# Optimization experiments

Hardware: AMD Instinct MI355X
Metric: run time of the kernel (lower is better)

## Reference

```python
import jax, jax.numpy as jnp
import numpy as np

# dims
N, E, B, T = 1024, 8192, 4, 8          # nodes, edges, batch, time steps
IN, HID, H, NCLASS = 64, 64, 4, 7      # in_dim, nhidden, heads, nclass
K = N - NCLASS + 1                     # output-head conv width
NEG, EPS = 0.2, 1e-5


def setup_inputs() -> dict:
    key = jax.random.key(0)
    ks = jax.random.split(key, 24)
    p = lambda i, shape: jax.random.normal(ks[i], shape, jnp.float32) * 0.05
    inputs = jax.random.normal(ks[0], (B, IN, T, N), jnp.float32)
    src = jax.random.randint(ks[1], (E,), 0, N, jnp.int32)
    dst = jnp.repeat(jnp.arange(N, dtype=jnp.int32), E // N)  # every node has in-degree 8
    return {
        "inputs": inputs, "src": src, "dst": dst,
        "W0": p(2, (H * HID, IN)), "al0": p(3, (H, HID)), "ar0": p(4, (H, HID)),
        "W1": p(5, (H * HID, H * HID)), "al1": p(6, (H, HID)), "ar1": p(7, (H, HID)),
        "W2": p(8, (H * 1, H * HID)), "al2": p(9, (H, 1)), "ar2": p(10, (H, 1)),
        "Wres2": p(11, (H * 1, H * HID)),
        # Outputlayer
        "tc1_w": p(12, (H, H, T)), "tc1_b": p(13, (H,)),
        "ln1_g": jnp.ones((N, H), jnp.float32), "ln1_b": jnp.zeros((N, H), jnp.float32),
        "tc2_w": p(14, (1, H)), "tc2_b": p(15, (1,)),
        "ln2_g": jnp.ones((N, 1), jnp.float32), "ln2_b": jnp.zeros((N, 1), jnp.float32),
        "fc_w": p(16, (K,)), "fc_b": p(17, (1,)),
    }


def _gat_conv(h, src, dst, W, al, ar, res=None, act=None):
    # h: (N,B,T,F) -> feat: (N,B,T,H,D)
    heads, d = al.shape
    feat = (h @ W.T).reshape(N, B, T, heads, d)
    el = jnp.einsum('nbthd,hd->nbth', feat, al)
    er = jnp.einsum('nbthd,hd->nbth', feat, ar)
    e = jax.nn.leaky_relu(el[src] + er[dst], NEG)           # (E,B,T,H)
    emax = jax.ops.segment_max(e, dst, num_segments=N)
    ex = jnp.exp(e - emax[dst])
    den = jax.ops.segment_sum(ex, dst, num_segments=N)
    a = ex / den[dst]                                        # edge softmax over incoming edges
    out = jax.ops.segment_sum(feat[src] * a[..., None], dst, num_segments=N)  # (N,B,T,H,D)
    if res is not None:
        out = out + res
    if act is not None:
        out = act(out)
    return out


def reference(inputs, src, dst,
              W0, al0, ar0, W1, al1, ar1, W2, al2, ar2, Wres2,
              tc1_w, tc1_b, ln1_g, ln1_b, tc2_w, tc2_b, ln2_g, ln2_b, fc_w, fc_b):
    # (B,IN,T,N) -> (N,B,T,IN) : transpose(0,3).transpose(1,3)
    h = jnp.transpose(inputs.astype(jnp.float32), (3, 0, 2, 1))
    h1 = _gat_conv(h, src, dst, W0, al0, ar0, act=jax.nn.elu).reshape(N, B, T, H * HID)
    h2 = _gat_conv(h1, src, dst, W1, al1, ar1,
                   res=h1.reshape(N, B, T, H, HID), act=jax.nn.elu).reshape(N, B, T, H * HID)
    res2 = (h2 @ Wres2.T).reshape(N, B, T, H, 1)
    o = _gat_conv(h2, src, dst, W2, al2, ar2, res=res2)      # (N,B,T,H,1)
    # transpose(1,3).transpose(0,3).squeeze(-1) -> (B,H,T,N)
    x = jnp.transpose(o[..., 0], (1, 3, 2, 0))

    # Outputlayer
    # tconv1: Conv2d(H->H, kernel (T,1)) collapses time -> (B,H,N)
    x1 = jnp.einsum('oht,bhtn->bon', tc1_w, x) + tc1_b[None, :, None]
    # ln1: LayerNorm over (N,H) of (B,1,N,H)
    z = jnp.transpose(x1, (0, 2, 1))                          # (B,N,H)
    mu = z.mean(axis=(1, 2), keepdims=True)
    var = z.var(axis=(1, 2), keepdims=True)
    z = (z - mu) / jnp.sqrt(var + EPS) * ln1_g + ln1_b
    x1 = jnp.transpose(z, (0, 2, 1))                          # (B,H,N)
    # tconv2: 1x1 conv H->1 -> (B,1,N)
    x2 = jnp.einsum('oh,bhn->bon', tc2_w, x1) + tc2_b[None, :, None]
    # ln2: LayerNorm over (N,1)
    mu = x2.mean(axis=2, keepdims=True)
    var = x2.var(axis=2, keepdims=True)
    x2 = (x2 - mu) / jnp.sqrt(var + EPS) * ln2_g[:, 0] + ln2_b[:, 0]
    # fc: Conv2d(1->1, kernel (1,K)) sliding over nodes -> (B,NCLASS)
    xc = x2[:, :, None, :]                                    # (B,1,1,N) NCHW
    w = fc_w[None, None, None, :]                             # (1,1,1,K) OIHW
    out = jax.lax.conv_general_dilated(xc, w, (1, 1), 'VALID') + fc_b[None, :, None, None]
    return out[:, 0, 0, :]                                    # (B, NCLASS)
```

## Files before the change

### kernel.cpp

```cpp
#include <hip/hip_runtime.h>
#include <math.h>

#define NEGS 0.2f
#define EPSF 1e-5f

typedef short s16x8 __attribute__((ext_vector_type(8)));
typedef float f32x4 __attribute__((ext_vector_type(4)));

__device__ __forceinline__ float b2f(unsigned short u) {
  union { unsigned int i; float f; } v; v.i = ((unsigned int)u) << 16; return v.f;
}
__device__ __forceinline__ unsigned short f2b(float f) {
  union { float f; unsigned int i; } v; v.f = f;
  unsigned int x = v.i;
  return (unsigned short)((x + 0x7fffu + ((x >> 16) & 1u)) >> 16);
}

__device__ __forceinline__ float block_reduce1024(float v, float* red) {
  #pragma unroll
  for (int o = 32; o > 0; o >>= 1) v += __shfl_down(v, o);
  __syncthreads();
  if ((threadIdx.x & 63) == 0) red[threadIdx.x >> 6] = v;
  __syncthreads();
  float s = 0.f;
  #pragma unroll
  for (int i = 0; i < 16; ++i) s += red[i];
  return s;
}

__global__ __launch_bounds__(256) void k_feat0(
    const float* __restrict__ inp, const float* __restrict__ W0,
    const float* __restrict__ W1, const float* __restrict__ al,
    const float* __restrict__ ar, unsigned short* __restrict__ feat,
    float* __restrict__ el, float* __restrict__ er,
    unsigned short* __restrict__ W1b)
{
  const int tid = threadIdx.x;
  if (blockIdx.x >= 512) {
    const int j = (blockIdx.x - 512) * 256 + tid;
    float4 w4 = *(const float4*)&W1[j*4];
    ushort4 o4; o4.x=f2b(w4.x); o4.y=f2b(w4.y); o4.z=f2b(w4.z); o4.w=f2b(w4.w);
    *(ushort4*)&W1b[j*4] = o4;
    return;
  }
  __shared__ __align__(16) unsigned short At[64][72];
  __shared__ __align__(16) unsigned short Lb[64*256];
  const int g  = blockIdx.x & 7;
  const int bt = g*4 + ((blockIdx.x >> 3) & 3);
  const int n0 = (blockIdx.x >> 5) * 64;
  const int b  = bt >> 3, t = bt & 7;
  const int w    = tid >> 6;
  const int lane = tid & 63;
  const int n16  = lane & 15;
  const int q    = lane >> 4;
  s16x8 bf[2][4];
  #pragma unroll
  for (int kc = 0; kc < 2; ++kc)
    #pragma unroll
    for (int ct = 0; ct < 4; ++ct) {
      const float* p = &W0[(size_t)((w*4 + ct)*16 + n16)*64 + kc*32 + q*8];
      float4 wa = *(const float4*)p;
      float4 wb = *(const float4*)(p + 4);
      s16x8 o;
      o[0]=(short)f2b(wa.x); o[1]=(short)f2b(wa.y); o[2]=(short)f2b(wa.z); o[3]=(short)f2b(wa.w);
      o[4]=(short)f2b(wb.x); o[5]=(short)f2b(wb.y); o[6]=(short)f2b(wb.z); o[7]=(short)f2b(wb.w);
      bf[kc][ct] = o;
    }
  {
    const int nn = tid & 63, cg = tid >> 6;
    #pragma unroll
    for (int c2 = 0; c2 < 8; ++c2) {
      int ch = (cg*8 + c2) * 2;
      float vx = inp[((size_t)(b*64 + ch  )*8 + t)*1024 + n0 + nn];
      float vy = inp[((size_t)(b*64 + ch+1)*8 + t)*1024 + n0 + nn];
      unsigned int pk = ((unsigned int)f2b(vy) << 16) | (unsigned int)f2b(vx);
      *(unsigned int*)&At[nn][ch] = pk;
    }
  }
  __syncthreads();
  f32x4 acc[4][4];
  #pragma unroll
  for (int rt = 0; rt < 4; ++rt)
    #pragma unroll
    for (int ct = 0; ct < 4; ++ct) acc[rt][ct] = (f32x4){0.f,0.f,0.f,0.f};
  #pragma unroll
  for (int kc = 0; kc < 2; ++kc) {
    s16x8 af[4];
    #pragma unroll
    for (int rt = 0; rt < 4; ++rt)
      af[rt] = *(const s16x8*)&At[rt*16 + n16][kc*32 + q*8];
    #pragma unroll
    for (int rt = 0; rt < 4; ++rt)
      #pragma unroll
      for (int ct = 0; ct < 4; ++ct)
        acc[rt][ct] = __builtin_amdgcn_mfma_f32_16x16x32_bf16(af[rt], bf[kc][ct], acc[rt][ct], 0, 0, 0);
  }
  float alv[4], arv[4];
  #pragma unroll
  for (int ct = 0; ct < 4; ++ct) {
    alv[ct] = al[w*64 + ct*16 + n16];
    arv[ct] = ar[w*64 + ct*16 + n16];
  }
  #pragma unroll
  for (int rt = 0; rt < 4; ++rt) {
    #pragma unroll
    for (int reg = 0; reg < 4; ++reg) {
      float pl = acc[rt][0][reg]*alv[0] + acc[rt][1][reg]*alv[1]
               + acc[rt][2][reg]*alv[2] + acc[rt][3][reg]*alv[3];
      float pr = acc[rt][0][reg]*arv[0] + acc[rt][1][reg]*arv[1]
               + acc[rt][2][reg]*arv[2] + acc[rt][3][reg]*arv[3];
      #pragma unroll
      for (int o = 1; o < 16; o <<= 1) { pl += __shfl_xor(pl, o); pr += __shfl_xor(pr, o); }
      if (n16 == 0) {
        int r = (n0 + rt*16 + q*4 + reg)*32 + bt;
        el[r*4 + w] = pl;
        er[r*4 + w] = pr;
      }
    }
  }
  #pragma unroll
  for (int rt = 0; rt < 4; ++rt)
    #pragma unroll
    for (int ct = 0; ct < 4; ++ct)
      #pragma unroll
      for (int reg = 0; reg < 4; ++reg)
        Lb[(rt*16 + q*4 + reg)*256 + w*64 + ct*16 + n16] = f2b(acc[rt][ct][reg]);
  __syncthreads();
  #pragma unroll
  for (int i = 0; i < 8; ++i) {
    int u = tid + i*256;
    int m = u >> 5, off = (u & 31) * 8;
    *(s16x8*)&feat[(size_t)((n0 + m)*32 + bt)*256 + off] = *(const s16x8*)&Lb[m*256 + off];
  }
}

__global__ __launch_bounds__(256, 4) void k_agg0_feat1(
    const unsigned short* __restrict__ feat0, const float* __restrict__ el0,
    const float* __restrict__ er0, const int* __restrict__ src,
    const unsigned short* __restrict__ W1b, const float* __restrict__ al,
    const float* __restrict__ ar, unsigned short* __restrict__ h1b,
    unsigned short* __restrict__ feat1, float* __restrict__ el1, float* __restrict__ er1)
{
  __shared__ float wsm[32][8][4];
  __shared__ int   ssm[32][8];
  __shared__ __align__(16) unsigned short smbuf[32*264];
  unsigned short (*At)[264] = (unsigned short(*)[264])smbuf;
  unsigned short *Lb = smbuf;
  const int tid = threadIdx.x;
  const int g     = blockIdx.x & 7;
  const int bt    = g*4 + ((blockIdx.x >> 3) & 3);
  const int nBase = (blockIdx.x >> 5) * 32;
  ((int*)ssm)[tid] = src[nBase*8 + tid];
  __syncthreads();
  if (tid < 128) {
    const int nl = tid >> 2, h = tid & 3;
    const int rn = (nBase + nl)*32 + bt;
    const float erv = er0[rn*4 + h];
    float e[8]; float mx = -1e30f;
    #pragma unroll
    for (int j = 0; j < 8; ++j) {
      float v = el0[(ssm[nl][j]*32 + bt)*4 + h] + erv;
      v = v >= 0.f ? v : NEGS * v;
      e[j] = v; mx = fmaxf(mx, v);
    }
    float den = 0.f;
    #pragma unroll
    for (int j = 0; j < 8; ++j) { e[j] = __expf(e[j] - mx); den += e[j]; }
    const float inv = 1.f / den;
    #pragma unroll
    for (int j = 0; j < 8; ++j) wsm[nl][j][h] = e[j] * inv;
  }
  __syncthreads();
  {
    const int hw2 = tid >> 5, l5 = tid & 31;
    const int c0 = l5 * 8, hh = l5 >> 3;
    #pragma unroll
    for (int p2 = 0; p2 < 2; ++p2) {
      const int nlA = p2*16 + hw2, nlB = nlA + 8;
      s16x8 vA[8], vB[8];
      #pragma unroll
      for (int j = 0; j < 8; ++j) {
        vA[j] = *(const s16x8*)&feat0[(size_t)(ssm[nlA][j]*32 + bt)*256 + c0];
        vB[j] = *(const s16x8*)&feat0[(size_t)(ssm[nlB][j]*32 + bt)*256 + c0];
      }
      asm volatile("" ::: "memory");
      float aA[8] = {0,0,0,0,0,0,0,0}, aB[8] = {0,0,0,0,0,0,0,0};
      #pragma unroll
      for (int j = 0; j < 8; ++j) {
        const float wA = wsm[nlA][j][hh], wB = wsm[nlB][j][hh];
        #pragma unroll
        for (int i = 0; i < 8; ++i) {
          aA[i] = fmaf(wA, b2f((unsigned short)vA[j][i]), aA[i]);
          aB[i] = fmaf(wB, b2f((unsigned short)vB[j][i]), aB[i]);
        }
      }
      s16x8 oA, oB;
      #pragma unroll
      for (int i = 0; i < 8; ++i) {
        float xA = aA[i] > 0.f ? aA[i] : expm1f(aA[i]);
        float xB = aB[i] > 0.f ? aB[i] : expm1f(aB[i]);
        oA[i] = (short)f2b(xA); oB[i] = (short)f2b(xB);
      }
      *(s16x8*)&At[nlA][c0] = oA;
      *(s16x8*)&At[nlB][c0] = oB;
      *(s16x8*)&h1b[(size_t)((nBase + nlA)*32 + bt)*256 + c0] = oA;
      *(s16x8*)&h1b[(size_t)((nBase + nlB)*32 + bt)*256 + c0] = oB;
    }
  }
  __syncthreads();
  const int w    = tid >> 6;
  const int lane = tid & 63;
  const int n16  = lane & 15;
  const int q    = lane >> 4;
  f32x4 acc[2][4];
  #pragma unroll
  for (int rt = 0; rt < 2; ++rt)
    #pragma unroll
    for (int ct = 0; ct < 4; ++ct) acc[rt][ct] = (f32x4){0.f,0.f,0.f,0.f};
  #pragma unroll
  for (int kc = 0; kc < 8; ++kc) {
    s16x8 af[2], bfr[4];
    #pragma unroll
    for (int rt = 0; rt < 2; ++rt)
      af[rt] = *(const s16x8*)&At[rt*16 + n16][kc*32 + q*8];
    #pragma unroll
    for (int ct = 0; ct < 4; ++ct)
      bfr[ct] = *(const s16x8*)&W1b[(size_t)((w*4 + ct)*16 + n16)*256 + kc*32 + q*8];
    #pragma unroll
    for (int rt = 0; rt < 2; ++rt)
      #pragma unroll
      for (int ct = 0; ct < 4; ++ct)
        acc[rt][ct] = __builtin_amdgcn_mfma_f32_16x16x32_bf16(af[rt], bfr[ct], acc[rt][ct], 0, 0, 0);
  }
  float alv[4], arv[4];
  #pragma unroll
  for (int ct = 0; ct < 4; ++ct) {
    alv[ct] = al[w*64 + ct*16 + n16];
    arv[ct] = ar[w*64 + ct*16 + n16];
  }
  #pragma unroll
  for (int rt = 0; rt < 2; ++rt) {
    #pragma unroll
    for (int reg = 0; reg < 4; ++reg) {
      float pl = acc[rt][0][reg]*alv[0] + acc[rt][1][reg]*alv[1]
               + acc[rt][2][reg]*alv[2] + acc[rt][3][reg]*alv[3];
      float pr = acc[rt][0][reg]*arv[0] + acc[rt][1][reg]*arv[1]
               + acc[rt][2][reg]*arv[2] + acc[rt][3][reg]*arv[3];
      #pragma unroll
      for (int o = 1; o < 16; o <<= 1) { pl += __shfl_xor(pl, o); pr += __shfl_xor(pr, o); }
      if (n16 == 0) {
        int r = (nBase + rt*16 + q*4 + reg)*32 + bt;
        el1[r*4 + w] = pl;
        er1[r*4 + w] = pr;
      }
    }
  }
  __syncthreads();
  #pragma unroll
  for (int rt = 0; rt < 2; ++rt)
    #pragma unroll
    for (int ct = 0; ct < 4; ++ct)
      #pragma unroll
      for (int reg = 0; reg < 4; ++reg)
        Lb[(rt*16 + q*4 + reg)*256 + w*64 + ct*16 + n16] = f2b(acc[rt][ct][reg]);
  __syncthreads();
  #pragma unroll
  for (int i = 0; i < 4; ++i) {
    int u = tid + i*256;
    int row = u >> 5, off = (u & 31) * 8;
    *(s16x8*)&feat1[(size_t)((nBase + row)*32 + bt)*256 + off] = *(const s16x8*)&Lb[row*256 + off];
  }
}

__global__ __launch_bounds__(256, 4) void k_agg1_proj(
    const unsigned short* __restrict__ feat1, const float* __restrict__ el,
    const float* __restrict__ er, const int* __restrict__ src,
    const unsigned short* __restrict__ h1b, const float* __restrict__ W2,
    const float* __restrict__ Wres2, float* __restrict__ feat2, float* __restrict__ res2)
{
  __shared__ float wsm[32][8][4];
  __shared__ int   ssm[32][8];
  __shared__ __align__(16) float Wp[8][256];
  const int tid = threadIdx.x;
  const int g     = blockIdx.x & 7;
  const int bt    = g*4 + ((blockIdx.x >> 3) & 3);
  const int nBase = (blockIdx.x >> 5) * 32;
  ((int*)ssm)[tid] = src[nBase*8 + tid];
  for (int j2 = tid; j2 < 2048; j2 += 256) {
    int o = j2 >> 8, k = j2 & 255;
    Wp[o][k] = (o < 4) ? W2[o*256 + k] : Wres2[(o-4)*256 + k];
  }
  __syncthreads();
  if (tid < 128) {
    const int nl = tid >> 2, h = tid & 3;
    const int rn = (nBase + nl)*32 + bt;
    const float erv = er[rn*4 + h];
    float e[8]; float mx = -1e30f;
    #pragma unroll
    for (int j = 0; j < 8; ++j) {
      float v = el[(ssm[nl][j]*32 + bt)*4 + h] + erv;
      v = v >= 0.f ? v : NEGS * v;
      e[j] = v; mx = fmaxf(mx, v);
    }
    float den = 0.f;
    #pragma unroll
    for (int j = 0; j < 8; ++j) { e[j] = __expf(e[j] - mx); den += e[j]; }
    const float inv = 1.f / den;
    #pragma unroll
    for (int j = 0; j < 8; ++j) wsm[nl][j][h] = e[j] * inv;
  }
  __syncthreads();
  const int hw2 = tid >> 5, l5 = tid & 31;
  const int c0 = l5 * 8, hh = l5 >> 3;
  #pragma unroll
  for (int p2 = 0; p2 < 2; ++p2) {
    const int nlA = p2*16 + hw2, nlB = nlA + 8;
    const int rnA = (nBase + nlA)*32 + bt, rnB = (nBase + nlB)*32 + bt;
    s16x8 vA[8], vB[8], rrA, rrB;
    rrA = *(const s16x8*)&h1b[(size_t)rnA*256 + c0];
    rrB = *(const s16x8*)&h1b[(size_t)rnB*256 + c0];
    #pragma unroll
    for (int j = 0; j < 8; ++j) {
      vA[j] = *(const s16x8*)&feat1[(size_t)(ssm[nlA][j]*32 + bt)*256 + c0];
      vB[j] = *(const s16x8*)&feat1[(size_t)(ssm[nlB][j]*32 + bt)*256 + c0];
    }
    asm volatile("" ::: "memory");
    float aA[8] = {0,0,0,0,0,0,0,0}, aB[8] = {0,0,0,0,0,0,0,0};
    #pragma unroll
    for (int j = 0; j < 8; ++j) {
      const float wA = wsm[nlA][j][hh], wB = wsm[nlB][j][hh];
      #pragma unroll
      for (int i = 0; i < 8; ++i) {
        aA[i] = fmaf(wA, b2f((unsigned short)vA[j][i]), aA[i]);
        aB[i] = fmaf(wB, b2f((unsigned short)vB[j][i]), aB[i]);
      }
    }
    #pragma unroll
    for (int i = 0; i < 8; ++i) {
      float xA = aA[i] + b2f((unsigned short)rrA[i]);
      float xB = aB[i] + b2f((unsigned short)rrB[i]);
      aA[i] = xA > 0.f ? xA : expm1f(xA);
      aB[i] = xB > 0.f ? xB : expm1f(xB);
    }
    #pragma unroll
    for (int o = 0; o < 8; ++o) {
      float4 wa = *(const float4*)&Wp[o][c0];
      float4 wb = *(const float4*)&Wp[o][c0 + 4];
      float pA = aA[0]*wa.x + aA[1]*wa.y + aA[2]*wa.z + aA[3]*wa.w
               + aA[4]*wb.x + aA[5]*wb.y + aA[6]*wb.z + aA[7]*wb.w;
      float pB = aB[0]*wa.x + aB[1]*wa.y + aB[2]*wa.z + aB[3]*wa.w
               + aB[4]*wb.x + aB[5]*wb.y + aB[6]*wb.z + aB[7]*wb.w;
      #pragma unroll
      for (int off = 1; off < 32; off <<= 1) {
        pA += __shfl_xor(pA, off);
        pB += __shfl_xor(pB, off);
      }
      if (l5 == 0) {
        if (o < 4) { feat2[rnA*4 + o] = pA; feat2[rnB*4 + o] = pB; }
        else       { res2[rnA*4 + (o-4)] = pA; res2[rnB*4 + (o-4)] = pB; }
      }
    }
  }
}

__global__ __launch_bounds__(128) void k_agg2(
    const float* __restrict__ feat2, const float* __restrict__ res2,
    const int* __restrict__ src, const float* __restrict__ al2,
    const float* __restrict__ ar2, const float* __restrict__ tc1w,
    const float* __restrict__ tc1b, float* __restrict__ x1)
{
  __shared__ float os[4][8][4];
  const int n = blockIdx.x;
  const int tid = threadIdx.x;
  const int b = tid >> 5, t = (tid >> 2) & 7, h = tid & 3;
  const int rn = n*32 + b*8 + t;
  const float av = al2[h], rv = ar2[h];
  const float erv = feat2[rn*4 + h] * rv;
  float f[8], e[8]; float m = -1e30f;
  #pragma unroll
  for (int j = 0; j < 8; ++j) {
    int s_ = src[n*8 + j];
    f[j] = feat2[(s_*32 + b*8 + t)*4 + h];
    float v = f[j]*av + erv;
    v = v >= 0.f ? v : NEGS * v;
    e[j] = v; m = fmaxf(m, v);
  }
  float den = 0.f, num = 0.f;
  #pragma unroll
  for (int j = 0; j < 8; ++j) { float ex = __expf(e[j]-m); den += ex; num = fmaf(ex, f[j], num); }
  os[b][t][h] = num/den + res2[rn*4 + h];
  __syncthreads();
  if (tid < 16) {
    int b2 = tid >> 2, o2 = tid & 3;
    float acc = tc1b[o2];
    #pragma unroll
    for (int hh = 0; hh < 4; ++hh)
      #pragma unroll
      for (int tt = 0; tt < 8; ++tt)
        acc = fmaf(tc1w[(o2*4 + hh)*8 + tt], os[b2][tt][hh], acc);
    x1[(b2*4 + o2)*1024 + n] = acc;
  }
}

__global__ __launch_bounds__(1024) void k_final(
    const float* __restrict__ x1, const float* __restrict__ ln1g,
    const float* __restrict__ ln1b, const float* __restrict__ tc2w,
    const float* __restrict__ tc2b, const float* __restrict__ ln2g,
    const float* __restrict__ ln2b, const float* __restrict__ fcw,
    const float* __restrict__ fcb, float* __restrict__ out)
{
  __shared__ float red[16];
  __shared__ float x2s[1024];
  const int b = blockIdx.x;
  const int tid = threadIdx.x;
  float s = 0.f, q = 0.f;
  for (int j = tid; j < 4096; j += 1024) {
    float v = x1[b*4096 + j];
    s += v; q += v*v;
  }
  float S = block_reduce1024(s, red);
  float Q = block_reduce1024(q, red);
  float mu  = S * (1.f/4096.f);
  float var = Q * (1.f/4096.f) - mu*mu;
  float inv = rsqrtf(var + EPSF);
  float tb = tc2b[0];
  const int nn = tid;
  float acc = tb;
  #pragma unroll
  for (int h = 0; h < 4; ++h) {
    float z = (x1[b*4096 + h*1024 + nn] - mu) * inv * ln1g[nn*4 + h] + ln1b[nn*4 + h];
    acc = fmaf(tc2w[h], z, acc);
  }
  float S2 = block_reduce1024(acc, red);
  float Q2 = block_reduce1024(acc*acc, red);
  float mu2  = S2 * (1.f/1024.f);
  float inv2 = rsqrtf(Q2 * (1.f/1024.f) - mu2*mu2 + EPSF);
  x2s[nn] = (acc - mu2) * inv2 * ln2g[nn] + ln2b[nn];
  __syncthreads();
  for (int c = 0; c < 7; ++c) {
    float p = (tid < 1018) ? x2s[c + tid] * fcw[tid] : 0.f;
    float P = block_reduce1024(p, red);
    if (tid == 0) out[b*7 + c] = P + fcb[0];
  }
}

extern "C" void kernel_launch(void* const* d_in, const int* in_sizes, int n_in,
                              void* d_out, int out_size, void* d_ws, size_t ws_size,
                              hipStream_t stream)
{
  const float* inp  = (const float*)d_in[0];
  const int*   src  = (const int*)  d_in[1];
  const float* W0   = (const float*)d_in[3];
  const float* al0  = (const float*)d_in[4];
  const float* ar0  = (const float*)d_in[5];
  const float* W1   = (const float*)d_in[6];
  const float* al1  = (const float*)d_in[7];
  const float* ar1  = (const float*)d_in[8];
  const float* W2   = (const float*)d_in[9];
  const float* al2  = (const float*)d_in[10];
  const float* ar2  = (const float*)d_in[11];
  const float* Wr2  = (const float*)d_in[12];
  const float* tc1w = (const float*)d_in[13];
  const float* tc1b = (const float*)d_in[14];
  const float* ln1g = (const float*)d_in[15];
  const float* ln1b = (const float*)d_in[16];
  const float* tc2w = (const float*)d_in[17];
  const float* tc2b = (const float*)d_in[18];
  const float* ln2g = (const float*)d_in[19];
  const float* ln2b = (const float*)d_in[20];
  const float* fcw  = (const float*)d_in[21];
  const float* fcb  = (const float*)d_in[22];
  float* out = (float*)d_out;

  unsigned short* W1b    = (unsigned short*)d_ws;
  unsigned short* featb0 = W1b    + 65536;
  unsigned short* featb1 = featb0 + 8388608;
  unsigned short* h1b    = featb1 + 8388608;
  float* el0   = (float*)(h1b + 8388608);
  float* er0   = el0   + 131072;
  float* el1   = er0   + 131072;
  float* er1   = el1   + 131072;
  float* feat2 = er1   + 131072;
  float* res2  = feat2 + 131072;
  float* x1    = res2  + 131072;

  k_feat0<<<dim3(576), dim3(256), 0, stream>>>(inp, W0, W1, al0, ar0,
                                               featb0, el0, er0, W1b);
  k_agg0_feat1<<<dim3(1024), dim3(256), 0, stream>>>(featb0, el0, er0, src, W1b, al1, ar1,
                                                     h1b, featb1, el1, er1);
  k_agg1_proj<<<dim3(1024), dim3(256), 0, stream>>>(featb1, el1, er1, src, h1b, W2, Wr2,
                                                    feat2, res2);
  k_agg2<<<dim3(1024), dim3(128), 0, stream>>>(feat2, res2, src, al2, ar2, tc1w, tc1b, x1);
  k_final<<<dim3(4), dim3(1024), 0, stream>>>(x1, ln1g, ln1b, tc2w, tc2b, ln2g, ln2b, fcw, fcb, out);
}
```

Measured before the change: 170.7 us.

## Aggregate before projecting in GAT layers and fold attention vectors into weights

```diff
diff --git a/kernel.cpp b/kernel.cpp
--- a/kernel.cpp
+++ b/kernel.cpp
@@ -15,6 +15,7 @@
   unsigned int x = v.i;
   return (unsigned short)((x + 0x7fffu + ((x >> 16) & 1u)) >> 16);
 }
+__device__ __forceinline__ float eluf(float x) { return x > 0.f ? x : expm1f(x); }
 
 __device__ __forceinline__ float block_reduce1024(float v, float* red) {
   #pragma unroll
@@ -28,138 +29,154 @@
   return s;
 }
 
-__global__ __launch_bounds__(256) void k_feat0(
+__global__ __launch_bounds__(256) void k_pre(
     const float* __restrict__ inp, const float* __restrict__ W0,
-    const float* __restrict__ W1, const float* __restrict__ al,
-    const float* __restrict__ ar, unsigned short* __restrict__ feat,
-    float* __restrict__ el, float* __restrict__ er,
-    unsigned short* __restrict__ W1b)
+    const float* __restrict__ W1, const float* __restrict__ al0,
+    const float* __restrict__ ar0, const float* __restrict__ al1,
+    const float* __restrict__ ar1, unsigned short* __restrict__ Xb,
+    unsigned short* __restrict__ W0b, unsigned short* __restrict__ W1b,
+    float* __restrict__ vl0g, float* __restrict__ vr0g,
+    float* __restrict__ vl1g, float* __restrict__ vr1g)
 {
   const int tid = threadIdx.x;
+  if (blockIdx.x == 576) {
+    float accl1[4] = {0,0,0,0}, accr1[4] = {0,0,0,0};
+    #pragma unroll
+    for (int h = 0; h < 4; ++h)
+      for (int d = 0; d < 64; ++d) {
+        float w = W1[(size_t)(h*64 + d)*256 + tid];
+        accl1[h] = fmaf(w, al1[h*64 + d], accl1[h]);
+        accr1[h] = fmaf(w, ar1[h*64 + d], accr1[h]);
+      }
+    #pragma unroll
+    for (int h = 0; h < 4; ++h) { vl1g[h*256 + tid] = accl1[h]; vr1g[h*256 + tid] = accr1[h]; }
+    if (tid < 64) {
+      float accl0[4] = {0,0,0,0}, accr0[4] = {0,0,0,0};
+      for (int h = 0; h < 4; ++h)
+        for (int d = 0; d < 64; ++d) {
+          float w = W0[(h*64 + d)*64 + tid];
+          accl0[h] = fmaf(w, al0[h*64 + d], accl0[h]);
+          accr0[h] = fmaf(w, ar0[h*64 + d], accr0[h]);
+        }
+      for (int h = 0; h < 4; ++h) { vl0g[h*64 + tid] = accl0[h]; vr0g[h*64 + tid] = accr0[h]; }
+    }
+    return;
+  }
   if (blockIdx.x >= 512) {
     const int j = (blockIdx.x - 512) * 256 + tid;
+    W0b[j] = f2b(W0[j]);
     float4 w4 = *(const float4*)&W1[j*4];
     ushort4 o4; o4.x=f2b(w4.x); o4.y=f2b(w4.y); o4.z=f2b(w4.z); o4.w=f2b(w4.w);
     *(ushort4*)&W1b[j*4] = o4;
     return;
   }
-  __shared__ __align__(16) unsigned short At[64][72];
-  __shared__ __align__(16) unsigned short Lb[64*256];
-  const int g  = blockIdx.x & 7;
-  const int bt = g*4 + ((blockIdx.x >> 3) & 3);
-  const int n0 = (blockIdx.x >> 5) * 64;
-  const int b  = bt >> 3, t = bt & 7;
-  const int w    = tid >> 6;
-  const int lane = tid & 63;
-  const int n16  = lane & 15;
-  const int q    = lane >> 4;
-  s16x8 bf[2][4];
-  #pragma unroll
-  for (int kc = 0; kc < 2; ++kc)
-    #pragma unroll
-    for (int ct = 0; ct < 4; ++ct) {
-      const float* p = &W0[(size_t)((w*4 + ct)*16 + n16)*64 + kc*32 + q*8];
-      float4 wa = *(const float4*)p;
-      float4 wb = *(const float4*)(p + 4);
-      s16x8 o;
-      o[0]=(short)f2b(wa.x); o[1]=(short)f2b(wa.y); o[2]=(short)f2b(wa.z); o[3]=(short)f2b(wa.w);
-      o[4]=(short)f2b(wb.x); o[5]=(short)f2b(wb.y); o[6]=(short)f2b(wb.z); o[7]=(short)f2b(wb.w);
-      bf[kc][ct] = o;
-    }
-  {
-    const int nn = tid & 63, cg = tid >> 6;
-    #pragma unroll
-    for (int c2 = 0; c2 < 8; ++c2) {
-      int ch = (cg*8 + c2) * 2;
-      float vx = inp[((size_t)(b*64 + ch  )*8 + t)*1024 + n0 + nn];
-      float vy = inp[((size_t)(b*64 + ch+1)*8 + t)*1024 + n0 + nn];
-      unsigned int pk = ((unsigned int)f2b(vy) << 16) | (unsigned int)f2b(vx);
-      *(unsigned int*)&At[nn][ch] = pk;
-    }
-  }
-  __syncthreads();
-  f32x4 acc[4][4];
-  #pragma unroll
-  for (int rt = 0; rt < 4; ++rt)
-    #pragma unroll
-    for (int ct = 0; ct < 4; ++ct) acc[rt][ct] = (f32x4){0.f,0.f,0.f,0.f};
-  #pragma unroll
-  for (int kc = 0; kc < 2; ++kc) {
-    s16x8 af[4];
-    #pragma unroll
-    for (int rt = 0; rt < 4; ++rt)
-      af[rt] = *(const s16x8*)&At[rt*16 + n16][kc*32 + q*8];
-    #pragma unroll
-    for (int rt = 0; rt < 4; ++rt)
-      #pragma unroll
-      for (int ct = 0; ct < 4; ++ct)
-        acc[rt][ct] = __builtin_amdgcn_mfma_f32_16x16x32_bf16(af[rt], bf[kc][ct], acc[rt][ct], 0, 0, 0);
-  }
-  float alv[4], arv[4];
-  #pragma unroll
-  for (int ct = 0; ct < 4; ++ct) {
-    alv[ct] = al[w*64 + ct*16 + n16];
-    arv[ct] = ar[w*64 + ct*16 + n16];
-  }
-  #pragma unroll
-  for (int rt = 0; rt < 4; ++rt) {
-    #pragma unroll
-    for (int reg = 0; reg < 4; ++reg) {
-      float pl = acc[rt][0][reg]*alv[0] + acc[rt][1][reg]*alv[1]
-               + acc[rt][2][reg]*alv[2] + acc[rt][3][reg]*alv[3];
-      float pr = acc[rt][0][reg]*arv[0] + acc[rt][1][reg]*arv[1]
-               + acc[rt][2][reg]*arv[2] + acc[rt][3][reg]*arv[3];
-      #pragma unroll
-      for (int o = 1; o < 16; o <<= 1) { pl += __shfl_xor(pl, o); pr += __shfl_xor(pr, o); }
-      if (n16 == 0) {
-        int r = (n0 + rt*16 + q*4 + reg)*32 + bt;
-        el[r*4 + w] = pl;
-        er[r*4 + w] = pr;
-      }
-    }
-  }
-  #pragma unroll
-  for (int rt = 0; rt < 4; ++rt)
-    #pragma unroll
-    for (int ct = 0; ct < 4; ++ct)
-      #pragma unroll
-      for (int reg = 0; reg < 4; ++reg)
-        Lb[(rt*16 + q*4 + reg)*256 + w*64 + ct*16 + n16] = f2b(acc[rt][ct][reg]);
-  __syncthreads();
-  #pragma unroll
-  for (int i = 0; i < 8; ++i) {
-    int u = tid + i*256;
-    int m = u >> 5, off = (u & 31) * 8;
-    *(s16x8*)&feat[(size_t)((n0 + m)*32 + bt)*256 + off] = *(const s16x8*)&Lb[m*256 + off];
-  }
-}
-
-__global__ __launch_bounds__(256, 4) void k_agg0_feat1(
-    const unsigned short* __restrict__ feat0, const float* __restrict__ el0,
-    const float* __restrict__ er0, const int* __restrict__ src,
-    const unsigned short* __restrict__ W1b, const float* __restrict__ al,
-    const float* __restrict__ ar, unsigned short* __restrict__ h1b,
-    unsigned short* __restrict__ feat1, float* __restrict__ el1, float* __restrict__ er1)
+  __shared__ float L[64][65];
+  const int blk = blockIdx.x;
+  const int n0 = (blk & 15) * 64;
+  const int t  = (blk >> 4) & 7;
+  const int b  = blk >> 7;
+  const int nn = tid & 63, ch0 = tid >> 6;
+  #pragma unroll
+  for (int ch = ch0; ch < 64; ch += 4)
+    L[ch][nn] = inp[((size_t)(b*64 + ch)*8 + t)*1024 + n0 + nn];
+  __syncthreads();
+  const int r = tid >> 2, ck = tid & 3;
+  s16x8 o0, o1;
+  #pragma unroll
+  for (int i = 0; i < 8; ++i) o0[i] = (short)f2b(L[ck*16 + i][r]);
+  #pragma unroll
+  for (int i = 0; i < 8; ++i) o1[i] = (short)f2b(L[ck*16 + 8 + i][r]);
+  const int row = (n0 + r)*32 + b*8 + t;
+  *(s16x8*)&Xb[(size_t)row*64 + ck*16]     = o0;
+  *(s16x8*)&Xb[(size_t)row*64 + ck*16 + 8] = o1;
+}
+
+__global__ __launch_bounds__(256) void k_l0(
+    const unsigned short* __restrict__ Xb, const int* __restrict__ src,
+    const unsigned short* __restrict__ W0b, const float* __restrict__ vl0g,
+    const float* __restrict__ vr0g, const float* __restrict__ vl1g,
+    const float* __restrict__ vr1g, unsigned short* __restrict__ h1b,
+    float* __restrict__ el1, float* __restrict__ er1)
 {
-  __shared__ float wsm[32][8][4];
   __shared__ int   ssm[32][8];
-  __shared__ __align__(16) unsigned short smbuf[32*264];
-  unsigned short (*At)[264] = (unsigned short(*)[264])smbuf;
-  unsigned short *Lb = smbuf;
+  __shared__ __align__(16) float vl0s[4][64], vr0s[4][64];
+  __shared__ __align__(16) float vl1s[4][256], vr1s[4][256];
+  __shared__ float er0s[32][4];
+  __shared__ float el0s[32][8][4];
+  __shared__ float a_lds[32][33];
+  __shared__ __align__(16) unsigned short x_lds[32][8][72];
+  __shared__ __align__(16) unsigned short At[4][32][72];
+  __shared__ float elpart[4][32][4], erpart[4][32][4];
   const int tid = threadIdx.x;
   const int g     = blockIdx.x & 7;
   const int bt    = g*4 + ((blockIdx.x >> 3) & 3);
   const int nBase = (blockIdx.x >> 5) * 32;
+
   ((int*)ssm)[tid] = src[nBase*8 + tid];
-  __syncthreads();
+  ((float4*)vl1s)[tid] = ((const float4*)vl1g)[tid];
+  ((float4*)vr1s)[tid] = ((const float4*)vr1g)[tid];
+  if (tid < 64) {
+    ((float4*)vl0s)[tid] = ((const float4*)vl0g)[tid];
+    ((float4*)vr0s)[tid] = ((const float4*)vr0g)[tid];
+  }
+  __syncthreads();
+
+  {
+    const int nl = tid >> 3, j = tid & 7;
+    const unsigned short* xp = Xb + (size_t)(ssm[nl][j]*32 + bt)*64;
+    s16x8 xr[8];
+    #pragma unroll
+    for (int i = 0; i < 8; ++i) xr[i] = *(const s16x8*)&xp[i*8];
+    s16x8 xo = *(const s16x8*)&Xb[(size_t)((nBase + nl)*32 + bt)*64 + j*8];
+    asm volatile("" ::: "memory");
+    #pragma unroll
+    for (int h = 0; h < 4; ++h) {
+      float s = 0.f;
+      #pragma unroll
+      for (int i = 0; i < 8; ++i) {
+        f32x4 va = *(const f32x4*)&vl0s[h][i*8];
+        f32x4 vb = *(const f32x4*)&vl0s[h][i*8 + 4];
+        s = fmaf(b2f((unsigned short)xr[i][0]), va[0], s);
+        s = fmaf(b2f((unsigned short)xr[i][1]), va[1], s);
+        s = fmaf(b2f((unsigned short)xr[i][2]), va[2], s);
+        s = fmaf(b2f((unsigned short)xr[i][3]), va[3], s);
+        s = fmaf(b2f((unsigned short)xr[i][4]), vb[0], s);
+        s = fmaf(b2f((unsigned short)xr[i][5]), vb[1], s);
+        s = fmaf(b2f((unsigned short)xr[i][6]), vb[2], s);
+        s = fmaf(b2f((unsigned short)xr[i][7]), vb[3], s);
+      }
+      el0s[nl][j][h] = s;
+    }
+    float erp[4];
+    #pragma unroll
+    for (int h = 0; h < 4; ++h) {
+      f32x4 va = *(const f32x4*)&vr0s[h][j*8];
+      f32x4 vb = *(const f32x4*)&vr0s[h][j*8 + 4];
+      float s = b2f((unsigned short)xo[0])*va[0] + b2f((unsigned short)xo[1])*va[1]
+              + b2f((unsigned short)xo[2])*va[2] + b2f((unsigned short)xo[3])*va[3]
+              + b2f((unsigned short)xo[4])*vb[0] + b2f((unsigned short)xo[5])*vb[1]
+              + b2f((unsigned short)xo[6])*vb[2] + b2f((unsigned short)xo[7])*vb[3];
+      erp[h] = s;
+    }
+    #pragma unroll
+    for (int o = 1; o < 8; o <<= 1)
+      #pragma unroll
+      for (int h = 0; h < 4; ++h) erp[h] += __shfl_xor(erp[h], o);
+    if (j == 0)
+      #pragma unroll
+      for (int h = 0; h < 4; ++h) er0s[nl][h] = erp[h];
+    #pragma unroll
+    for (int i = 0; i < 8; ++i) *(s16x8*)&x_lds[nl][j][i*8] = xr[i];
+  }
+  __syncthreads();
+
   if (tid < 128) {
     const int nl = tid >> 2, h = tid & 3;
-    const int rn = (nBase + nl)*32 + bt;
-    const float erv = er0[rn*4 + h];
+    const float erv = er0s[nl][h];
     float e[8]; float mx = -1e30f;
     #pragma unroll
     for (int j = 0; j < 8; ++j) {
-      float v = el0[(ssm[nl][j]*32 + bt)*4 + h] + erv;
+      float v = el0s[nl][j][h] + erv;
       v = v >= 0.f ? v : NEGS * v;
       e[j] = v; mx = fmaxf(mx, v);
     }
@@ -168,46 +185,33 @@
     for (int j = 0; j < 8; ++j) { e[j] = __expf(e[j] - mx); den += e[j]; }
     const float inv = 1.f / den;
     #pragma unroll
-    for (int j = 0; j < 8; ++j) wsm[nl][j][h] = e[j] * inv;
-  }
-  __syncthreads();
-  {
-    const int hw2 = tid >> 5, l5 = tid & 31;
-    const int c0 = l5 * 8, hh = l5 >> 3;
-    #pragma unroll
-    for (int p2 = 0; p2 < 2; ++p2) {
-      const int nlA = p2*16 + hw2, nlB = nlA + 8;
-      s16x8 vA[8], vB[8];
+    for (int j = 0; j < 8; ++j) a_lds[nl][j*4 + h] = e[j] * inv;
+  }
+  __syncthreads();
+
+  {
+    const int nl = tid >> 3, ci = tid & 7;
+    s16x8 xv[8];
+    #pragma unroll
+    for (int j = 0; j < 8; ++j) xv[j] = *(const s16x8*)&x_lds[nl][j][ci*8];
+    #pragma unroll
+    for (int h = 0; h < 4; ++h) {
+      float acc8[8] = {0,0,0,0,0,0,0,0};
       #pragma unroll
       for (int j = 0; j < 8; ++j) {
-        vA[j] = *(const s16x8*)&feat0[(size_t)(ssm[nlA][j]*32 + bt)*256 + c0];
-        vB[j] = *(const s16x8*)&feat0[(size_t)(ssm[nlB][j]*32 + bt)*256 + c0];
-      }
-      asm volatile("" ::: "memory");
-      float aA[8] = {0,0,0,0,0,0,0,0}, aB[8] = {0,0,0,0,0,0,0,0};
-      #pragma unroll
-      for (int j = 0; j < 8; ++j) {
-        const float wA = wsm[nlA][j][hh], wB = wsm[nlB][j][hh];
-        #pragma unroll
-        for (int i = 0; i < 8; ++i) {
-          aA[i] = fmaf(wA, b2f((unsigned short)vA[j][i]), aA[i]);
-          aB[i] = fmaf(wB, b2f((unsigned short)vB[j][i]), aB[i]);
-        }
-      }
-      s16x8 oA, oB;
-      #pragma unroll
-      for (int i = 0; i < 8; ++i) {
-        float xA = aA[i] > 0.f ? aA[i] : expm1f(aA[i]);
-        float xB = aB[i] > 0.f ? aB[i] : expm1f(aB[i]);
-        oA[i] = (short)f2b(xA); oB[i] = (short)f2b(xB);
-      }
-      *(s16x8*)&At[nlA][c0] = oA;
-      *(s16x8*)&At[nlB][c0] = oB;
-      *(s16x8*)&h1b[(size_t)((nBase + nlA)*32 + bt)*256 + c0] = oA;
-      *(s16x8*)&h1b[(size_t)((nBase + nlB)*32 + bt)*256 + c0] = oB;
-    }
-  }
-  __syncthreads();
+        const float wa = a_lds[nl][j*4 + h];
+        #pragma unroll
+        for (int e = 0; e < 8; ++e)
+          acc8[e] = fmaf(wa, b2f((unsigned short)xv[j][e]), acc8[e]);
+      }
+      s16x8 o;
+      #pragma unroll
+      for (int e = 0; e < 8; ++e) o[e] = (short)f2b(acc8[e]);
+      *(s16x8*)&At[h][nl][ci*8] = o;
+    }
+  }
+  __syncthreads();
+
   const int w    = tid >> 6;
   const int lane = tid & 63;
   const int n16  = lane & 15;
@@ -218,69 +222,92 @@
     #pragma unroll
     for (int ct = 0; ct < 4; ++ct) acc[rt][ct] = (f32x4){0.f,0.f,0.f,0.f};
   #pragma unroll
-  for (int kc = 0; kc < 8; ++kc) {
+  for (int kc = 0; kc < 2; ++kc) {
     s16x8 af[2], bfr[4];
     #pragma unroll
     for (int rt = 0; rt < 2; ++rt)
-      af[rt] = *(const s16x8*)&At[rt*16 + n16][kc*32 + q*8];
+      af[rt] = *(const s16x8*)&At[w][rt*16 + n16][kc*32 + q*8];
     #pragma unroll
     for (int ct = 0; ct < 4; ++ct)
-      bfr[ct] = *(const s16x8*)&W1b[(size_t)((w*4 + ct)*16 + n16)*256 + kc*32 + q*8];
+      bfr[ct] = *(const s16x8*)&W0b[(size_t)((w*4 + ct)*16 + n16)*64 + kc*32 + q*8];
     #pragma unroll
     for (int rt = 0; rt < 2; ++rt)
       #pragma unroll
       for (int ct = 0; ct < 4; ++ct)
         acc[rt][ct] = __builtin_amdgcn_mfma_f32_16x16x32_bf16(af[rt], bfr[ct], acc[rt][ct], 0, 0, 0);
   }
-  float alv[4], arv[4];
-  #pragma unroll
-  for (int ct = 0; ct < 4; ++ct) {
-    alv[ct] = al[w*64 + ct*16 + n16];
-    arv[ct] = ar[w*64 + ct*16 + n16];
-  }
-  #pragma unroll
-  for (int rt = 0; rt < 2; ++rt) {
-    #pragma unroll
-    for (int reg = 0; reg < 4; ++reg) {
-      float pl = acc[rt][0][reg]*alv[0] + acc[rt][1][reg]*alv[1]
-               + acc[rt][2][reg]*alv[2] + acc[rt][3][reg]*alv[3];
-      float pr = acc[rt][0][reg]*arv[0] + acc[rt][1][reg]*arv[1]
-               + acc[rt][2][reg]*arv[2] + acc[rt][3][reg]*arv[3];
-      #pragma unroll
-      for (int o = 1; o < 16; o <<= 1) { pl += __shfl_xor(pl, o); pr += __shfl_xor(pr, o); }
-      if (n16 == 0) {
-        int r = (nBase + rt*16 + q*4 + reg)*32 + bt;
-        el1[r*4 + w] = pl;
-        er1[r*4 + w] = pr;
-      }
-    }
-  }
-  __syncthreads();
-  #pragma unroll
-  for (int rt = 0; rt < 2; ++rt)
-    #pragma unroll
-    for (int ct = 0; ct < 4; ++ct)
-      #pragma unroll
-      for (int reg = 0; reg < 4; ++reg)
-        Lb[(rt*16 + q*4 + reg)*256 + w*64 + ct*16 + n16] = f2b(acc[rt][ct][reg]);
-  __syncthreads();
-  #pragma unroll
-  for (int i = 0; i < 4; ++i) {
-    int u = tid + i*256;
-    int row = u >> 5, off = (u & 31) * 8;
-    *(s16x8*)&feat1[(size_t)((nBase + row)*32 + bt)*256 + off] = *(const s16x8*)&Lb[row*256 + off];
-  }
-}
-
-__global__ __launch_bounds__(256, 4) void k_agg1_proj(
-    const unsigned short* __restrict__ feat1, const float* __restrict__ el,
+
+  {
+    float vl1v[4][4], vr1v[4][4];
+    #pragma unroll
+    for (int h = 0; h < 4; ++h)
+      #pragma unroll
+      for (int ct = 0; ct < 4; ++ct) {
+        vl1v[h][ct] = vl1s[h][w*64 + ct*16 + n16];
+        vr1v[h][ct] = vr1s[h][w*64 + ct*16 + n16];
+      }
+    unsigned short* Hb = &x_lds[0][0][0];
+    #pragma unroll
+    for (int rt = 0; rt < 2; ++rt) {
+      #pragma unroll
+      for (int reg = 0; reg < 4; ++reg) {
+        const int row = rt*16 + q*4 + reg;
+        float hv[4];
+        #pragma unroll
+        for (int ct = 0; ct < 4; ++ct) hv[ct] = eluf(acc[rt][ct][reg]);
+        float ep[4], rp[4];
+        #pragma unroll
+        for (int h = 0; h < 4; ++h) {
+          ep[h] = hv[0]*vl1v[h][0] + hv[1]*vl1v[h][1] + hv[2]*vl1v[h][2] + hv[3]*vl1v[h][3];
+          rp[h] = hv[0]*vr1v[h][0] + hv[1]*vr1v[h][1] + hv[2]*vr1v[h][2] + hv[3]*vr1v[h][3];
+        }
+        #pragma unroll
+        for (int o = 1; o < 16; o <<= 1)
+          #pragma unroll
+          for (int h = 0; h < 4; ++h) { ep[h] += __shfl_xor(ep[h], o); rp[h] += __shfl_xor(rp[h], o); }
+        if (n16 == 0)
+          #pragma unroll
+          for (int h = 0; h < 4; ++h) { elpart[w][row][h] = ep[h]; erpart[w][row][h] = rp[h]; }
+        #pragma unroll
+        for (int ct = 0; ct < 4; ++ct)
+          Hb[row*256 + w*64 + ct*16 + n16] = f2b(hv[ct]);
+      }
+    }
+  }
+  __syncthreads();
+
+  {
+    const unsigned short* Hb = &x_lds[0][0][0];
+    #pragma unroll
+    for (int i = 0; i < 4; ++i) {
+      int u = tid + i*256;
+      int row = u >> 5, off = (u & 31) * 8;
+      *(s16x8*)&h1b[(size_t)((nBase + row)*32 + bt)*256 + off] = *(const s16x8*)&Hb[row*256 + off];
+    }
+    if (tid < 128) {
+      const int row = tid >> 2, h = tid & 3;
+      float se = 0.f, sr = 0.f;
+      #pragma unroll
+      for (int ww = 0; ww < 4; ++ww) { se += elpart[ww][row][h]; sr += erpart[ww][row][h]; }
+      const int r = (nBase + row)*32 + bt;
+      el1[r*4 + h] = se;
+      er1[r*4 + h] = sr;
+    }
+  }
+}
+
+__global__ __launch_bounds__(256, 3) void k_l1(
+    const unsigned short* __restrict__ h1b, const float* __restrict__ el,
     const float* __restrict__ er, const int* __restrict__ src,
-    const unsigned short* __restrict__ h1b, const float* __restrict__ W2,
+    const unsigned short* __restrict__ W1b, const float* __restrict__ W2,
     const float* __restrict__ Wres2, float* __restrict__ feat2, float* __restrict__ res2)
 {
   __shared__ float wsm[32][8][4];
   __shared__ int   ssm[32][8];
   __shared__ __align__(16) float Wp[8][256];
+  __shared__ __align__(16) unsigned short At[32][264];
+  __shared__ __align__(16) unsigned short own[32][264];
+  __shared__ float pp[4][32][8];
   const int tid = threadIdx.x;
   const int g     = blockIdx.x & 7;
   const int bt    = g*4 + ((blockIdx.x >> 3) & 3);
@@ -310,56 +337,105 @@
     for (int j = 0; j < 8; ++j) wsm[nl][j][h] = e[j] * inv;
   }
   __syncthreads();
-  const int hw2 = tid >> 5, l5 = tid & 31;
-  const int c0 = l5 * 8, hh = l5 >> 3;
-  #pragma unroll
-  for (int p2 = 0; p2 < 2; ++p2) {
-    const int nlA = p2*16 + hw2, nlB = nlA + 8;
-    const int rnA = (nBase + nlA)*32 + bt, rnB = (nBase + nlB)*32 + bt;
-    s16x8 vA[8], vB[8], rrA, rrB;
-    rrA = *(const s16x8*)&h1b[(size_t)rnA*256 + c0];
-    rrB = *(const s16x8*)&h1b[(size_t)rnB*256 + c0];
-    #pragma unroll
-    for (int j = 0; j < 8; ++j) {
-      vA[j] = *(const s16x8*)&feat1[(size_t)(ssm[nlA][j]*32 + bt)*256 + c0];
-      vB[j] = *(const s16x8*)&feat1[(size_t)(ssm[nlB][j]*32 + bt)*256 + c0];
-    }
-    asm volatile("" ::: "memory");
-    float aA[8] = {0,0,0,0,0,0,0,0}, aB[8] = {0,0,0,0,0,0,0,0};
-    #pragma unroll
-    for (int j = 0; j < 8; ++j) {
-      const float wA = wsm[nlA][j][hh], wB = wsm[nlB][j][hh];
-      #pragma unroll
-      for (int i = 0; i < 8; ++i) {
-        aA[i] = fmaf(wA, b2f((unsigned short)vA[j][i]), aA[i]);
-        aB[i] = fmaf(wB, b2f((unsigned short)vB[j][i]), aB[i]);
-      }
-    }
-    #pragma unroll
-    for (int i = 0; i < 8; ++i) {
-      float xA = aA[i] + b2f((unsigned short)rrA[i]);
-      float xB = aB[i] + b2f((unsigned short)rrB[i]);
-      aA[i] = xA > 0.f ? xA : expm1f(xA);
-      aB[i] = xB > 0.f ? xB : expm1f(xB);
-    }
-    #pragma unroll
-    for (int o = 0; o < 8; ++o) {
-      float4 wa = *(const float4*)&Wp[o][c0];
-      float4 wb = *(const float4*)&Wp[o][c0 + 4];
-      float pA = aA[0]*wa.x + aA[1]*wa.y + aA[2]*wa.z + aA[3]*wa.w
-               + aA[4]*wb.x + aA[5]*wb.y + aA[6]*wb.z + aA[7]*wb.w;
-      float pB = aB[0]*wa.x + aB[1]*wa.y + aB[2]*wa.z + aB[3]*wa.w
-               + aB[4]*wb.x + aB[5]*wb.y + aB[6]*wb.z + aB[7]*wb.w;
-      #pragma unroll
-      for (int off = 1; off < 32; off <<= 1) {
-        pA += __shfl_xor(pA, off);
-        pB += __shfl_xor(pB, off);
-      }
-      if (l5 == 0) {
-        if (o < 4) { feat2[rnA*4 + o] = pA; feat2[rnB*4 + o] = pB; }
-        else       { res2[rnA*4 + (o-4)] = pA; res2[rnB*4 + (o-4)] = pB; }
-      }
-    }
+  {
+    const int hw2 = tid >> 5, l5 = tid & 31;
+    const int c0 = l5 * 8, hh = l5 >> 3;
+    #pragma unroll
+    for (int p2 = 0; p2 < 2; ++p2) {
+      const int nlA = p2*16 + hw2, nlB = nlA + 8;
+      s16x8 vA[8], vB[8];
+      #pragma unroll
+      for (int j = 0; j < 8; ++j) {
+        vA[j] = *(const s16x8*)&h1b[(size_t)(ssm[nlA][j]*32 + bt)*256 + c0];
+        vB[j] = *(const s16x8*)&h1b[(size_t)(ssm[nlB][j]*32 + bt)*256 + c0];
+      }
+      asm volatile("" ::: "memory");
+      float aA[8] = {0,0,0,0,0,0,0,0}, aB[8] = {0,0,0,0,0,0,0,0};
+      #pragma unroll
+      for (int j = 0; j < 8; ++j) {
+        const float wA = wsm[nlA][j][hh], wB = wsm[nlB][j][hh];
+        #pragma unroll
+        for (int i = 0; i < 8; ++i) {
+          aA[i] = fmaf(wA, b2f((unsigned short)vA[j][i]), aA[i]);
+          aB[i] = fmaf(wB, b2f((unsigned short)vB[j][i]), aB[i]);
+        }
+      }
+      s16x8 oA, oB;
+      #pragma unroll
+      for (int i = 0; i < 8; ++i) { oA[i] = (short)f2b(aA[i]); oB[i] = (short)f2b(aB[i]); }
+      *(s16x8*)&At[nlA][c0] = oA;
+      *(s16x8*)&At[nlB][c0] = oB;
+    }
+    #pragma unroll
+    for (int i = 0; i < 4; ++i) {
+      int u = tid + i*256;
+      int row = u >> 5, off = (u & 31) * 8;
+      *(s16x8*)&own[row][off] = *(const s16x8*)&h1b[(size_t)((nBase + row)*32 + bt)*256 + off];
+    }
+  }
+  __syncthreads();
+  const int w    = tid >> 6;
+  const int lane = tid & 63;
+  const int n16  = lane & 15;
+  const int q    = lane >> 4;
+  f32x4 acc[2][4];
+  #pragma unroll
+  for (int rt = 0; rt < 2; ++rt)
+    #pragma unroll
+    for (int ct = 0; ct < 4; ++ct) acc[rt][ct] = (f32x4){0.f,0.f,0.f,0.f};
+  #pragma unroll
+  for (int kc = 0; kc < 8; ++kc) {
+    s16x8 af[2], bfr[4];
+    #pragma unroll
+    for (int rt = 0; rt < 2; ++rt)
+      af[rt] = *(const s16x8*)&At[rt*16 + n16][kc*32 + q*8];
+    #pragma unroll
+    for (int ct = 0; ct < 4; ++ct)
+      bfr[ct] = *(const s16x8*)&W1b[(size_t)((w*4 + ct)*16 + n16)*256 + kc*32 + q*8];
+    #pragma unroll
+    for (int rt = 0; rt < 2; ++rt)
+      #pragma unroll
+      for (int ct = 0; ct < 4; ++ct)
+        acc[rt][ct] = __builtin_amdgcn_mfma_f32_16x16x32_bf16(af[rt], bfr[ct], acc[rt][ct], 0, 0, 0);
+  }
+  {
+    float wpv[8][4];
+    #pragma unroll
+    for (int o = 0; o < 8; ++o)
+      #pragma unroll
+      for (int ct = 0; ct < 4; ++ct) wpv[o][ct] = Wp[o][w*64 + ct*16 + n16];
+    #pragma unroll
+    for (int rt = 0; rt < 2; ++rt) {
+      #pragma unroll
+      for (int reg = 0; reg < 4; ++reg) {
+        const int row = rt*16 + q*4 + reg;
+        float h2[4];
+        #pragma unroll
+        for (int ct = 0; ct < 4; ++ct) {
+          float v = acc[rt][ct][reg] + b2f(own[row][w*64 + ct*16 + n16]);
+          h2[ct] = eluf(v);
+        }
+        float pf[8];
+        #pragma unroll
+        for (int o = 0; o < 8; ++o)
+          pf[o] = h2[0]*wpv[o][0] + h2[1]*wpv[o][1] + h2[2]*wpv[o][2] + h2[3]*wpv[o][3];
+        #pragma unroll
+        for (int of = 1; of < 16; of <<= 1)
+          #pragma unroll
+          for (int o = 0; o < 8; ++o) pf[o] += __shfl_xor(pf[o], of);
+        if (n16 == 0)
+          #pragma unroll
+          for (int o = 0; o < 8; ++o) pp[w][row][o] = pf[o];
+      }
+    }
+  }
+  __syncthreads();
+  {
+    const int row = tid >> 3, o = tid & 7;
+    float s = pp[0][row][o] + pp[1][row][o] + pp[2][row][o] + pp[3][row][o];
+    const int rn = (nBase + row)*32 + bt;
+    if (o < 4) feat2[rn*4 + o] = s;
+    else       res2[rn*4 + (o-4)] = s;
   }
 }
 
@@ -472,24 +548,26 @@
   const float* fcb  = (const float*)d_in[22];
   float* out = (float*)d_out;
 
-  unsigned short* W1b    = (unsigned short*)d_ws;
-  unsigned short* featb0 = W1b    + 65536;
-  unsigned short* featb1 = featb0 + 8388608;
-  unsigned short* h1b    = featb1 + 8388608;
-  float* el0   = (float*)(h1b + 8388608);
-  float* er0   = el0   + 131072;
-  float* el1   = er0   + 131072;
-  float* er1   = el1   + 131072;
-  float* feat2 = er1   + 131072;
+  unsigned short* Xb   = (unsigned short*)d_ws;
+  unsigned short* W0b  = Xb  + 2097152;
+  unsigned short* W1b  = W0b + 16384;
+  unsigned short* h1b  = W1b + 65536;
+  float* vl0g  = (float*)(h1b + 8388608);
+  float* vr0g  = vl0g + 256;
+  float* vl1g  = vr0g + 256;
+  float* vr1g  = vl1g + 1024;
+  float* el1   = vr1g + 1024;
+  float* er1   = el1 + 131072;
+  float* feat2 = er1 + 131072;
   float* res2  = feat2 + 131072;
-  float* x1    = res2  + 131072;
-
-  k_feat0<<<dim3(576), dim3(256), 0, stream>>>(inp, W0, W1, al0, ar0,
-                                               featb0, el0, er0, W1b);
-  k_agg0_feat1<<<dim3(1024), dim3(256), 0, stream>>>(featb0, el0, er0, src, W1b, al1, ar1,
-                                                     h1b, featb1, el1, er1);
-  k_agg1_proj<<<dim3(1024), dim3(256), 0, stream>>>(featb1, el1, er1, src, h1b, W2, Wr2,
-                                                    feat2, res2);
+  float* x1    = res2 + 131072;
+
+  k_pre<<<dim3(577), dim3(256), 0, stream>>>(inp, W0, W1, al0, ar0, al1, ar1,
+                                             Xb, W0b, W1b, vl0g, vr0g, vl1g, vr1g);
+  k_l0<<<dim3(1024), dim3(256), 0, stream>>>(Xb, src, W0b, vl0g, vr0g, vl1g, vr1g,
+                                             h1b, el1, er1);
+  k_l1<<<dim3(1024), dim3(256), 0, stream>>>(h1b, el1, er1, src, W1b, W2, Wr2,
+                                             feat2, res2);
   k_agg2<<<dim3(1024), dim3(128), 0, stream>>>(feat2, res2, src, al2, ar2, tc1w, tc1b, x1);
   k_final<<<dim3(4), dim3(1024), 0, stream>>>(x1, ln1g, ln1b, tc2w, tc2b, ln2g, ln2b, fcw, fcb, out);
 }
```

Measured after the change: 220.1 us. 28.9% more time.
